# Kernel tuning notes

Measured on AMD Instinct MI355X. Metric: run time of the kernel, lower is better.

The kernel has to match this reference:

```python
import jax, jax.numpy as jnp
import numpy as np


def _conv1x1(x, W, b):
    # x: [B,C,H,W] (NCHW), W: [out,in] (1x1 conv kernel), b: [out]
    return jnp.einsum('bchw,oc->bohw', x, W) + b[None, :, None, None]


def setup_inputs() -> dict:
    key = jax.random.key(0)
    ks = jax.random.split(key, 12)
    B, C, H, W = 8, 256, 64, 64
    s = 1.0 / np.sqrt(C)
    x = jax.random.normal(ks[0], (B, C, H, W), dtype=jnp.float32)
    mask = jnp.round(jax.random.uniform(ks[1], (B, 1, H, W), dtype=jnp.float32))
    Wq = jax.random.normal(ks[2], (C, C), dtype=jnp.float32) * s
    bq = jax.random.normal(ks[3], (C,), dtype=jnp.float32) * 0.01
    Wk = jax.random.normal(ks[4], (C, C), dtype=jnp.float32) * s
    bk = jax.random.normal(ks[5], (C,), dtype=jnp.float32) * 0.01
    Wv = jax.random.normal(ks[6], (C, C), dtype=jnp.float32) * s
    bv = jax.random.normal(ks[7], (C,), dtype=jnp.float32) * 0.01
    Wo = jax.random.normal(ks[8], (C, C), dtype=jnp.float32) * s
    bo = jax.random.normal(ks[9], (C,), dtype=jnp.float32) * 0.01
    gamma = jnp.zeros((1,), dtype=jnp.float32)
    return {"input": x, "mask": mask, "Wq": Wq, "bq": bq, "Wk": Wk, "bk": bk,
            "Wv": Wv, "bv": bv, "Wo": Wo, "bo": bo, "gamma": gamma}


def reference(input, mask, Wq, bq, Wk, bk, Wv, bv, Wo, bo, gamma):
    B, C, H, W = input.shape
    # mask spatial size matches input -> no avg_pool branch (pre_feat is None)
    feat_f = input * mask            # foreground features -> queries
    feat_b = input * (1.0 - mask)    # background features -> keys/values
    q = _conv1x1(feat_f, Wq, bq).reshape(B, C, -1)   # [B,C,N]
    k = _conv1x1(feat_b, Wk, bk).reshape(B, C, -1)   # [B,C,N]
    v = _conv1x1(feat_b, Wv, bv).reshape(B, C, -1)   # [B,C,N]
    # scores[b,n,m] = q[:,n]^T k[:,m]  (no scaling, matching the torch code)
    scores = jnp.einsum('bcn,bcm->bnm', q, k)        # [B,N,N]
    attn = jax.nn.softmax(scores, axis=-1)
    out = jnp.einsum('bnm,bcm->bcn', attn, v).reshape(B, C, H, W)
    out = _conv1x1(out, Wo, bo)
    return out + gamma * input
```

## Files before the change

kernel.cpp:

```cpp
#include <hip/hip_runtime.h>

#define CC 256
#define NN 4096
#define NB 8
#define NM ((size_t)CC * NN)

typedef _Float16 f16;
typedef f16 f16x4 __attribute__((ext_vector_type(4)));
typedef f16 f16x8 __attribute__((ext_vector_type(8)));
typedef float f32x4 __attribute__((ext_vector_type(4)));
typedef unsigned int u32;

#define GLD16(gp, lp) __builtin_amdgcn_global_load_lds( \
    (const __attribute__((address_space(1))) u32*)(const void*)(gp), \
    (__attribute__((address_space(3))) u32*)(void*)(lp), 16, 0, 0)

__global__ __launch_bounds__(256) void wprep_kernel(
    const float* __restrict__ Wq, const float* __restrict__ Wk,
    const float* __restrict__ Wv, f16* __restrict__ w16)
{
    int i = (blockIdx.x * 256 + threadIdx.x) * 4;
    float4 a = *(const float4*)(Wq + i);
    float4 b = *(const float4*)(Wk + i);
    float4 c = *(const float4*)(Wv + i);
    f16x4 ha, hb, hc;
    ha[0]=(f16)a.x; ha[1]=(f16)a.y; ha[2]=(f16)a.z; ha[3]=(f16)a.w;
    hb[0]=(f16)b.x; hb[1]=(f16)b.y; hb[2]=(f16)b.z; hb[3]=(f16)b.w;
    hc[0]=(f16)c.x; hc[1]=(f16)c.y; hc[2]=(f16)c.z; hc[3]=(f16)c.w;
    *(f16x4*)(w16 + i)           = ha;
    *(f16x4*)(w16 + 65536 + i)   = hb;
    *(f16x4*)(w16 + 131072 + i)  = hc;
}

__global__ __launch_bounds__(256) void mask_scan_kernel(
    const float* __restrict__ mask, int* __restrict__ posm, int* __restrict__ counts)
{
    const int b = blockIdx.x;
    const int t = threadIdx.x;
    const int lane = t & 63, w = t >> 6;
    __shared__ int wsum[4];
    const float* mp = mask + (size_t)b * NN;
    int* pp = posm + (size_t)b * NN;

    int loc[16], cnt = 0;
#pragma unroll
    for (int i = 0; i < 16; ++i) {
        loc[i] = cnt;
        cnt += (mp[t * 16 + i] == 0.0f) ? 1 : 0;
    }
    int inc = cnt;
#pragma unroll
    for (int d = 1; d < 64; d <<= 1) {
        int v = __shfl_up(inc, d, 64);
        if (lane >= d) inc += v;
    }
    if (lane == 63) wsum[w] = inc;
    int exc = inc - cnt;
    __syncthreads();
    int base = exc;
    for (int i = 0; i < w; ++i) base += wsum[i];
#pragma unroll
    for (int i = 0; i < 16; ++i)
        pp[t * 16 + i] = (mp[t * 16 + i] == 0.0f) ? (base + loc[i]) : -1;
    if (t == 0) counts[b] = wsum[0] + wsum[1] + wsum[2] + wsum[3];
}

__global__ __launch_bounds__(256, 2) void proj_fused_kernel(
    const float* __restrict__ x, const float* __restrict__ mask,
    const f16* __restrict__ w16, const float* __restrict__ bq,
    const float* __restrict__ bk, const float* __restrict__ bv,
    f16* __restrict__ wsh, const int* __restrict__ posm,
    const int* __restrict__ counts, int b0)
{
    __shared__ f16x8 xf[2048];
    __shared__ f16x8 xb[2048];

    const int t = threadIdx.x;
    const int lane = t & 63, w = t >> 6;
    const int l16 = lane & 15, quad = lane >> 4;
    const int slot = blockIdx.x;
    const int b = b0 + slot;
    const int n0 = blockIdx.y * 64;
    const float* xp = x + (size_t)b * NM;
    f16* base = wsh + (size_t)slot * 4 * NM;
    const int* pom = posm + (size_t)b * NN;

    float mf  = mask[(size_t)b * NN + n0 + lane];
    float mbk = 1.0f - mf;
#pragma unroll
    for (int i = 0; i < 8; ++i) {
        int cb = w * 8 + i;
        const float* col = xp + (size_t)cb * 8 * NN + n0 + lane;
        f16x8 vf, vb;
#pragma unroll
        for (int u = 0; u < 8; ++u) {
            float xv = col[(size_t)u * NN];
            vf[u] = (f16)(xv * mf);
            vb[u] = (f16)(xv * mbk);
        }
        int unit = ((cb >> 2) * 4 + (lane >> 4)) * 64 + (cb & 3) * 16 + (lane & 15);
        xf[unit] = vf;
        xb[unit] = vb;
    }
    __syncthreads();

#pragma unroll
    for (int pr = 0; pr < 6; ++pr) {
        int j0  = w * 12 + pr * 2;
        int p   = j0 >> 4;
        int oc0 = j0 & 15;
        const f16* Wp     = w16 + (size_t)p * 65536;
        const float* bias = (p == 0) ? bq : (p == 1) ? bk : bv;
        const f16x8* bt   = (p == 0) ? xf : xb;

        f16x8 wf[2][8];
#pragma unroll
        for (int h = 0; h < 2; ++h) {
            const f16* wrow = Wp + (size_t)((oc0 + h) * 16 + l16) * CC + quad * 8;
#pragma unroll
            for (int kc = 0; kc < 8; ++kc)
                wf[h][kc] = *(const f16x8*)(wrow + kc * 32);
        }
        f32x4 acc[2][4];
#pragma unroll
        for (int h = 0; h < 2; ++h)
#pragma unroll
            for (int nc = 0; nc < 4; ++nc) acc[h][nc] = (f32x4){0.f, 0.f, 0.f, 0.f};
#pragma unroll
        for (int nc = 0; nc < 4; ++nc)
#pragma unroll
            for (int kc = 0; kc < 8; ++kc) {
                f16x8 bf = bt[(kc * 4 + nc) * 64 + lane];
                acc[0][nc] = __builtin_amdgcn_mfma_f32_16x16x32_f16(wf[0][kc], bf, acc[0][nc], 0, 0, 0);
                acc[1][nc] = __builtin_amdgcn_mfma_f32_16x16x32_f16(wf[1][kc], bf, acc[1][nc], 0, 0, 0);
            }
#pragma unroll
        for (int h = 0; h < 2; ++h) {
            int oc = oc0 + h;
            float bvv[4];
#pragma unroll
            for (int r = 0; r < 4; ++r) bvv[r] = bias[oc * 16 + quad * 4 + r];
            if (p == 2) {
                f16* vpl = base + 2 * NM;
#pragma unroll
                for (int nc = 0; nc < 4; ++nc) {
                    int cp = pom[n0 + nc * 16 + l16];
                    if (cp >= 0) {
#pragma unroll
                        for (int r = 0; r < 4; ++r)
                            vpl[(size_t)(oc * 16 + quad * 4 + r) * NN + cp] =
                                (f16)(acc[h][nc][r] + bvv[r]);
                    }
                }
            } else if (p == 1) {
                f16* kpl = base + NM;
#pragma unroll
                for (int nc = 0; nc < 4; ++nc) {
                    int cp = pom[n0 + nc * 16 + l16];
                    if (cp >= 0) {
                        f16x4 pk;
#pragma unroll
                        for (int r = 0; r < 4; ++r) pk[r] = (f16)(acc[h][nc][r] + bvv[r]);
                        *(f16x4*)(kpl + (size_t)cp * CC + oc * 16 + quad * 4) = pk;
                    }
                }
            } else {
                f16* qpl = base;
#pragma unroll
                for (int nc = 0; nc < 4; ++nc) {
                    f16x4 pk;
#pragma unroll
                    for (int r = 0; r < 4; ++r) pk[r] = (f16)(acc[h][nc][r] + bvv[r]);
                    *(f16x4*)(qpl + (size_t)(n0 + nc * 16 + l16) * CC + oc * 16 + quad * 4) = pk;
                }
            }
        }
    }

    if (blockIdx.y == 0) {
        int Fb = counts[b];
        int Mp = (Fb + 31) & ~31;
        int pad = Mp - Fb;
        if (pad > 0) {
            f16* kpl = base + NM;
            f16* vpl = base + 2 * NM;
            f16x8 z8;
#pragma unroll
            for (int i = 0; i < 8; ++i) z8[i] = (f16)0.0f;
            for (int idx = t; idx < pad * 32; idx += 256)
                *(f16x8*)(kpl + (size_t)(Fb + idx / 32) * CC + (idx & 31) * 8) = z8;
            for (int idx = t; idx < pad * CC; idx += 256)
                vpl[(size_t)(idx / pad) * NN + Fb + (idx % pad)] = (f16)0.0f;
        }
    }
}

__global__ __launch_bounds__(256, 2) void flash_kernel(
    f16* __restrict__ wsh, const float* __restrict__ bk,
    const float* __restrict__ bv, const int* __restrict__ counts, int b0)
{
    __shared__ f16x8 klds[2][1024];
    __shared__ f16x8 vlds[2][1024];
    __shared__ f16 pbuf[4][16 * 40];

    const int t    = threadIdx.x;
    const int w    = t >> 6;
    const int lane = t & 63;
    const int l16  = lane & 15;
    const int quad = lane >> 4;
    const int slot = blockIdx.x;
    const int n0   = blockIdx.y * 64;

    f16* base = wsh + (size_t)slot * 4 * NM;
    const f16* qt = base;
    const f16* kt = base + NM;
    const f16* vp = base + 2 * NM;
    f16* op       = base + 3 * NM;

    const int Fb = counts[b0 + slot];
    const int nt = (Fb + 31) >> 5;

    int koff[4], voff[4];
#pragma unroll
    for (int i = 0; i < 4; ++i) {
        int u = i * 256 + t;
        koff[i] = (((u >> 9) & 1) * 16 + (u & 15)) * CC
                + ((u >> 6) & 7) * 32 + ((u >> 4) & 3) * 8;
        voff[i] = ((u >> 6) * 16 + (u & 15)) * NN + ((u >> 4) & 3) * 8;
    }

#define ISSUE(m0_, b_) do {                                                     \
    _Pragma("unroll")                                                           \
    for (int i_ = 0; i_ < 4; ++i_)                                              \
        GLD16(kt + (size_t)(m0_) * CC + koff[i_],                               \
              (f16*)&klds[b_][i_ * 256 + w * 64]);                              \
    _Pragma("unroll")                                                           \
    for (int i_ = 0; i_ < 4; ++i_)                                              \
        GLD16(vp + (size_t)(m0_) + voff[i_],                                    \
              (f16*)&vlds[b_][i_ * 256 + w * 64]);                              \
} while (0)

    const int nrow = n0 + w * 16 + l16;
    f16x8 qf[8];
#pragma unroll
    for (int kc = 0; kc < 8; ++kc)
        qf[kc] = *(const f16x8*)(qt + (size_t)nrow * CC + kc * 32 + quad * 8);
#pragma unroll
    for (int kc = 0; kc < 8; ++kc)
        asm volatile("" :: "v"(qf[kc]));
    asm volatile("s_waitcnt vmcnt(0)" ::: "memory");

    f32x4 oacc[17];
#pragma unroll
    for (int i = 0; i < 17; ++i) oacc[i] = (f32x4){0.f, 0.f, 0.f, 0.f};
    float M[4] = {-3.0e38f, -3.0e38f, -3.0e38f, -3.0e38f};

    f16* pw = &pbuf[w][0];
    f16x8 ones;
#pragma unroll
    for (int i = 0; i < 8; ++i) ones[i] = (f16)1.0f;

    if (nt > 0) ISSUE(0, 0);
    int cur = 0;

    for (int it = 0; it < nt; ++it) {
        if (it + 1 < nt) {
            ISSUE((it + 1) * 32, cur ^ 1);
            asm volatile("s_waitcnt vmcnt(8)" ::: "memory");
        } else {
            asm volatile("s_waitcnt vmcnt(0)" ::: "memory");
        }
        __builtin_amdgcn_s_barrier();
        asm volatile("" ::: "memory");

        f32x4 s[2];
        s[0] = (f32x4){0.f, 0.f, 0.f, 0.f};
        s[1] = (f32x4){0.f, 0.f, 0.f, 0.f};
        __builtin_amdgcn_s_setprio(1);
#pragma unroll
        for (int kc = 0; kc < 8; ++kc) {
            f16x8 k0 = klds[cur][kc * 64 + lane];
            f16x8 k1 = klds[cur][(8 + kc) * 64 + lane];
            s[0] = __builtin_amdgcn_mfma_f32_16x16x32_f16(qf[kc], k0, s[0], 0, 0, 0);
            s[1] = __builtin_amdgcn_mfma_f32_16x16x32_f16(qf[kc], k1, s[1], 0, 0, 0);
        }
        __builtin_amdgcn_s_setprio(0);

        if (((it + 1) << 5) > Fb) {
#pragma unroll
            for (int ms = 0; ms < 2; ++ms)
                if (it * 32 + ms * 16 + l16 >= Fb) {
#pragma unroll
                    for (int r = 0; r < 4; ++r) s[ms][r] = -3.0e38f;
                }
        }

        bool up = false;
#pragma unroll
        for (int ms = 0; ms < 2; ++ms)
#pragma unroll
            for (int r = 0; r < 4; ++r) up |= (s[ms][r] > M[r] + 8.0f);
        if (__any(up)) {
            float alpha[4];
#pragma unroll
            for (int r = 0; r < 4; ++r) {
                float tm = fmaxf(s[0][r], s[1][r]);
                tm = fmaxf(tm, __shfl_xor(tm, 1, 64));
                tm = fmaxf(tm, __shfl_xor(tm, 2, 64));
                tm = fmaxf(tm, __shfl_xor(tm, 4, 64));
                tm = fmaxf(tm, __shfl_xor(tm, 8, 64));
                float Mn = fmaxf(M[r], tm);
                alpha[r] = __expf(M[r] - Mn);
                M[r] = Mn;
            }
#pragma unroll
            for (int cs = 0; cs < 17; ++cs)
#pragma unroll
                for (int r = 0; r < 4; ++r) oacc[cs][r] *= alpha[r];
        }
#pragma unroll
        for (int ms = 0; ms < 2; ++ms)
#pragma unroll
            for (int r = 0; r < 4; ++r)
                pw[(quad * 4 + r) * 40 + ms * 16 + l16] = (f16)__expf(s[ms][r] - M[r]);
        asm volatile("s_waitcnt lgkmcnt(0)" ::: "memory");
        f16x8 pf = *(const f16x8*)(pw + l16 * 40 + quad * 8);

        __builtin_amdgcn_s_setprio(1);
#pragma unroll
        for (int cs = 0; cs < 16; ++cs) {
            f16x8 vf = vlds[cur][cs * 64 + lane];
            oacc[cs] = __builtin_amdgcn_mfma_f32_16x16x32_f16(pf, vf, oacc[cs], 0, 0, 0);
        }
        oacc[16] = __builtin_amdgcn_mfma_f32_16x16x32_f16(pf, ones, oacc[16], 0, 0, 0);
        __builtin_amdgcn_s_setprio(0);

        asm volatile("" ::: "memory");
        __builtin_amdgcn_s_barrier();
        cur ^= 1;
    }
    asm volatile("s_waitcnt vmcnt(0)" ::: "memory");

    {
        float cn = 0.f;
#pragma unroll
        for (int kc = 0; kc < 8; ++kc) {
            const float* bkp = bk + kc * 32 + quad * 8;
#pragma unroll
            for (int j = 0; j < 8; ++j)
                cn += (float)qf[kc][j] * bkp[j];
        }
        cn += __shfl_xor(cn, 16, 64);
        cn += __shfl_xor(cn, 32, 64);
        const float Ff = (float)(NN - Fb);
        float aw[4], wv[4];
#pragma unroll
        for (int r = 0; r < 4; ++r) {
            float cr = __shfl(cn, quad * 4 + r, 64);
            float Mn = fmaxf(M[r], cr);
            aw[r] = __expf(M[r] - Mn);
            wv[r] = Ff * __expf(cr - Mn);
            M[r] = Mn;
        }
#pragma unroll
        for (int cs = 0; cs < 16; ++cs) {
            float bvc = bv[cs * 16 + l16];
#pragma unroll
            for (int r = 0; r < 4; ++r)
                oacc[cs][r] = oacc[cs][r] * aw[r] + wv[r] * bvc;
        }
#pragma unroll
        for (int r = 0; r < 4; ++r)
            oacc[16][r] = oacc[16][r] * aw[r] + wv[r];
    }

    float inv[4];
#pragma unroll
    for (int r = 0; r < 4; ++r) inv[r] = 1.0f / oacc[16][r];
#pragma unroll
    for (int cs = 0; cs < 16; ++cs)
#pragma unroll
        for (int r = 0; r < 4; ++r)
            op[(size_t)(cs * 16 + l16) * NN + n0 + w * 16 + quad * 4 + r] =
                (f16)(oacc[cs][r] * inv[r]);
#undef ISSUE
}

__global__ __launch_bounds__(256, 2) void final_kernel(
    const f16* __restrict__ wsh, const float* __restrict__ Wo,
    const float* __restrict__ bo, const float* __restrict__ x,
    const float* __restrict__ gamma, float* __restrict__ outall, int b0)
{
    __shared__ f16x8 ot[2048];

    const int t = threadIdx.x;
    const int lane = t & 63, w = t >> 6;
    const int l16 = lane & 15, quad = lane >> 4;
    const int slot = blockIdx.x;
    const int b = b0 + slot;
    const int n0 = blockIdx.y * 64;
    const f16* O = wsh + ((size_t)slot * 4 + 3) * NM;
    const float* xp = x + (size_t)b * NM;
    float* outp = outall + (size_t)b * NM;

#pragma unroll
    for (int i = 0; i < 8; ++i) {
        int cb = w * 8 + i;
        const f16* col = O + (size_t)cb * 8 * NN + n0 + lane;
        f16x8 v;
#pragma unroll
        for (int u = 0; u < 8; ++u) v[u] = col[(size_t)u * NN];
        ot[((cb >> 2) * 4 + (lane >> 4)) * 64 + (cb & 3) * 16 + (lane & 15)] = v;
    }
    __syncthreads();

    float g = gamma[0];
#pragma unroll
    for (int pr = 0; pr < 2; ++pr) {
        int oc0 = w * 4 + pr * 2;
        f16x8 wf[2][8];
#pragma unroll
        for (int h = 0; h < 2; ++h) {
            const float* wrow = Wo + (size_t)((oc0 + h) * 16 + l16) * CC + quad * 8;
#pragma unroll
            for (int kc = 0; kc < 8; ++kc) {
                float4 a = *(const float4*)(wrow + kc * 32);
                float4 c = *(const float4*)(wrow + kc * 32 + 4);
                f16x8 f;
                f[0] = (f16)a.x; f[1] = (f16)a.y; f[2] = (f16)a.z; f[3] = (f16)a.w;
                f[4] = (f16)c.x; f[5] = (f16)c.y; f[6] = (f16)c.z; f[7] = (f16)c.w;
                wf[h][kc] = f;
            }
        }
        f32x4 acc[2][4];
#pragma unroll
        for (int h = 0; h < 2; ++h)
#pragma unroll
            for (int nc = 0; nc < 4; ++nc) acc[h][nc] = (f32x4){0.f, 0.f, 0.f, 0.f};
#pragma unroll
        for (int nc = 0; nc < 4; ++nc)
#pragma unroll
            for (int kc = 0; kc < 8; ++kc) {
                f16x8 bf = ot[(kc * 4 + nc) * 64 + lane];
                acc[0][nc] = __builtin_amdgcn_mfma_f32_16x16x32_f16(wf[0][kc], bf, acc[0][nc], 0, 0, 0);
                acc[1][nc] = __builtin_amdgcn_mfma_f32_16x16x32_f16(wf[1][kc], bf, acc[1][nc], 0, 0, 0);
            }
#pragma unroll
        for (int h = 0; h < 2; ++h) {
            int oc = oc0 + h;
            float bvv[4];
#pragma unroll
            for (int r = 0; r < 4; ++r) bvv[r] = bo[oc * 16 + quad * 4 + r];
#pragma unroll
            for (int nc = 0; nc < 4; ++nc)
#pragma unroll
                for (int r = 0; r < 4; ++r) {
                    size_t o = oc * 16 + quad * 4 + r;
                    size_t n = n0 + nc * 16 + l16;
                    outp[o * NN + n] = acc[h][nc][r] + bvv[r] + g * xp[o * NN + n];
                }
        }
    }
}

__global__ __launch_bounds__(256) void ones_kernel(float* __restrict__ out, int total)
{
    for (int i = blockIdx.x * 256 + threadIdx.x; i < total; i += gridDim.x * 256)
        out[i] = 1.0f;
}

extern "C" void kernel_launch(void* const* d_in, const int* in_sizes, int n_in,
                              void* d_out, int out_size, void* d_ws, size_t ws_size,
                              hipStream_t stream)
{
    const float* x     = (const float*)d_in[0];
    const float* mask  = (const float*)d_in[1];
    const float* Wq    = (const float*)d_in[2];
    const float* bq    = (const float*)d_in[3];
    const float* Wk    = (const float*)d_in[4];
    const float* bk    = (const float*)d_in[5];
    const float* Wv    = (const float*)d_in[6];
    const float* bv    = (const float*)d_in[7];
    const float* Wo    = (const float*)d_in[8];
    const float* bo    = (const float*)d_in[9];
    const float* gamma = (const float*)d_in[10];
    float* out = (float*)d_out;

    const size_t slot_bytes = 4 * NM * sizeof(f16);
    f16* wsh = (f16*)d_ws;
    int nb = (int)(ws_size / slot_bytes);
    if (nb < 1) {
        ones_kernel<<<2048, 256, 0, stream>>>(out, out_size);
        return;
    }
    if (nb > NB) nb = NB;

    int* counts = (int*)(out + out_size) - 64;
    int* posm   = counts - NB * NN;
    f16* w16    = (f16*)posm - 3 * 65536;
    mask_scan_kernel<<<NB, 256, 0, stream>>>(mask, posm, counts);
    wprep_kernel<<<64, 256, 0, stream>>>(Wq, Wk, Wv, w16);

    for (int b0 = 0; b0 < NB; b0 += nb) {
        int nbc = NB - b0; if (nbc > nb) nbc = nb;
        dim3 gT(nbc, NN / 64);
        proj_fused_kernel<<<gT, 256, 0, stream>>>(x, mask, w16, bq, bk, bv,
                                                  wsh, posm, counts, b0);
        flash_kernel<<<gT, 256, 0, stream>>>(wsh, bk, bv, counts, b0);
        final_kernel<<<gT, 256, 0, stream>>>(wsh, Wo, bo, x, gamma, out, b0);
    }
}
```

Measured before the change: 310.8 us.

## Fuse output 1x1 projection into flash attention epilogue via LDS

The flash kernel now writes its normalized fp16 attention output tile into the shared-memory K buffers instead of global memory. It then runs the Wo projection, bias and gamma residual in the same block, which removes the separate final kernel and the global write and read of the O plane. Wo is pre-converted to fp16 once in the weight-prep kernel. The scratch data (fp16 weights, mask positions, counts) moves from the tail of the output buffer into the now-unused O plane of the workspace. This raises register and LDS pressure in the flash kernel and relies on the LDS reuse being synchronized correctly.

```diff
diff --git a/kernel.cpp b/kernel.cpp
--- a/kernel.cpp
+++ b/kernel.cpp
@@ -17,19 +17,23 @@
 
 __global__ __launch_bounds__(256) void wprep_kernel(
     const float* __restrict__ Wq, const float* __restrict__ Wk,
-    const float* __restrict__ Wv, f16* __restrict__ w16)
+    const float* __restrict__ Wv, const float* __restrict__ Wo,
+    f16* __restrict__ w16)
 {
     int i = (blockIdx.x * 256 + threadIdx.x) * 4;
     float4 a = *(const float4*)(Wq + i);
     float4 b = *(const float4*)(Wk + i);
     float4 c = *(const float4*)(Wv + i);
-    f16x4 ha, hb, hc;
+    float4 d = *(const float4*)(Wo + i);
+    f16x4 ha, hb, hc, hd;
     ha[0]=(f16)a.x; ha[1]=(f16)a.y; ha[2]=(f16)a.z; ha[3]=(f16)a.w;
     hb[0]=(f16)b.x; hb[1]=(f16)b.y; hb[2]=(f16)b.z; hb[3]=(f16)b.w;
     hc[0]=(f16)c.x; hc[1]=(f16)c.y; hc[2]=(f16)c.z; hc[3]=(f16)c.w;
-    *(f16x4*)(w16 + i)           = ha;
-    *(f16x4*)(w16 + 65536 + i)   = hb;
-    *(f16x4*)(w16 + 131072 + i)  = hc;
+    hd[0]=(f16)d.x; hd[1]=(f16)d.y; hd[2]=(f16)d.z; hd[3]=(f16)d.w;
+    *(f16x4*)(w16 + i)            = ha;
+    *(f16x4*)(w16 + 65536 + i)    = hb;
+    *(f16x4*)(w16 + 131072 + i)   = hc;
+    *(f16x4*)(w16 + 196608 + i)   = hd;
 }
 
 __global__ __launch_bounds__(256) void mask_scan_kernel(
@@ -197,7 +201,9 @@
 
 __global__ __launch_bounds__(256, 2) void flash_kernel(
     f16* __restrict__ wsh, const float* __restrict__ bk,
-    const float* __restrict__ bv, const int* __restrict__ counts, int b0)
+    const float* __restrict__ bv, const float* __restrict__ bo,
+    const float* __restrict__ x, const float* __restrict__ gamma,
+    float* __restrict__ outall, int b0)
 {
     __shared__ f16x8 klds[2][1024];
     __shared__ f16x8 vlds[2][1024];
@@ -215,9 +221,12 @@
     const f16* qt = base;
     const f16* kt = base + NM;
     const f16* vp = base + 2 * NM;
-    f16* op       = base + 3 * NM;
-
-    const int Fb = counts[b0 + slot];
+
+    const f16* wo16 = wsh + 3 * NM + (size_t)3 * 65536;
+    const int* counts = (const int*)(wsh + 3 * NM + (size_t)4 * 65536) + NB * NN;
+
+    const int b = b0 + slot;
+    const int Fb = counts[b];
     const int nt = (Fb + 31) >> 5;
 
     int koff[4], voff[4];
@@ -377,43 +386,22 @@
     float inv[4];
 #pragma unroll
     for (int r = 0; r < 4; ++r) inv[r] = 1.0f / oacc[16][r];
-#pragma unroll
-    for (int cs = 0; cs < 16; ++cs)
+
+    f16* otf = (f16*)&klds[0][0];
+#pragma unroll
+    for (int cs = 0; cs < 16; ++cs) {
+        int cb = cs * 2 + (l16 >> 3);
+        int ubase = ((cb >> 2) * 4 + w) * 64 + (cb & 3) * 16 + quad * 4;
+        int j = l16 & 7;
 #pragma unroll
         for (int r = 0; r < 4; ++r)
-            op[(size_t)(cs * 16 + l16) * NN + n0 + w * 16 + quad * 4 + r] =
-                (f16)(oacc[cs][r] * inv[r]);
-#undef ISSUE
-}
-
-__global__ __launch_bounds__(256, 2) void final_kernel(
-    const f16* __restrict__ wsh, const float* __restrict__ Wo,
-    const float* __restrict__ bo, const float* __restrict__ x,
-    const float* __restrict__ gamma, float* __restrict__ outall, int b0)
-{
-    __shared__ f16x8 ot[2048];
-
-    const int t = threadIdx.x;
-    const int lane = t & 63, w = t >> 6;
-    const int l16 = lane & 15, quad = lane >> 4;
-    const int slot = blockIdx.x;
-    const int b = b0 + slot;
-    const int n0 = blockIdx.y * 64;
-    const f16* O = wsh + ((size_t)slot * 4 + 3) * NM;
+            otf[(ubase + r) * 8 + j] = (f16)(oacc[cs][r] * inv[r]);
+    }
+    __syncthreads();
+
     const float* xp = x + (size_t)b * NM;
     float* outp = outall + (size_t)b * NM;
-
-#pragma unroll
-    for (int i = 0; i < 8; ++i) {
-        int cb = w * 8 + i;
-        const f16* col = O + (size_t)cb * 8 * NN + n0 + lane;
-        f16x8 v;
-#pragma unroll
-        for (int u = 0; u < 8; ++u) v[u] = col[(size_t)u * NN];
-        ot[((cb >> 2) * 4 + (lane >> 4)) * 64 + (cb & 3) * 16 + (lane & 15)] = v;
-    }
-    __syncthreads();
-
+    const f16x8* ot = (const f16x8*)otf;
     float g = gamma[0];
 #pragma unroll
     for (int pr = 0; pr < 2; ++pr) {
@@ -421,16 +409,10 @@
         f16x8 wf[2][8];
 #pragma unroll
         for (int h = 0; h < 2; ++h) {
-            const float* wrow = Wo + (size_t)((oc0 + h) * 16 + l16) * CC + quad * 8;
-#pragma unroll
-            for (int kc = 0; kc < 8; ++kc) {
-                float4 a = *(const float4*)(wrow + kc * 32);
-                float4 c = *(const float4*)(wrow + kc * 32 + 4);
-                f16x8 f;
-                f[0] = (f16)a.x; f[1] = (f16)a.y; f[2] = (f16)a.z; f[3] = (f16)a.w;
-                f[4] = (f16)c.x; f[5] = (f16)c.y; f[6] = (f16)c.z; f[7] = (f16)c.w;
-                wf[h][kc] = f;
-            }
+            const f16* wrow = wo16 + (size_t)((oc0 + h) * 16 + l16) * CC + quad * 8;
+#pragma unroll
+            for (int kc = 0; kc < 8; ++kc)
+                wf[h][kc] = *(const f16x8*)(wrow + kc * 32);
         }
         f32x4 acc[2][4];
 #pragma unroll
@@ -461,6 +443,7 @@
                 }
         }
     }
+#undef ISSUE
 }
 
 __global__ __launch_bounds__(256) void ones_kernel(float* __restrict__ out, int total)
@@ -495,18 +478,18 @@
     }
     if (nb > NB) nb = NB;
 
-    int* counts = (int*)(out + out_size) - 64;
-    int* posm   = counts - NB * NN;
-    f16* w16    = (f16*)posm - 3 * 65536;
+    f16* scr = wsh + 3 * NM;
+    f16* w16 = scr;
+    int* posm = (int*)(scr + (size_t)4 * 65536);
+    int* counts = posm + NB * NN;
     mask_scan_kernel<<<NB, 256, 0, stream>>>(mask, posm, counts);
-    wprep_kernel<<<64, 256, 0, stream>>>(Wq, Wk, Wv, w16);
+    wprep_kernel<<<64, 256, 0, stream>>>(Wq, Wk, Wv, Wo, w16);
 
     for (int b0 = 0; b0 < NB; b0 += nb) {
         int nbc = NB - b0; if (nbc > nb) nbc = nb;
         dim3 gT(nbc, NN / 64);
         proj_fused_kernel<<<gT, 256, 0, stream>>>(x, mask, w16, bq, bk, bv,
                                                   wsh, posm, counts, b0);
-        flash_kernel<<<gT, 256, 0, stream>>>(wsh, bk, bv, counts, b0);
-        final_kernel<<<gT, 256, 0, stream>>>(wsh, Wo, bo, x, gamma, out, b0);
-    }
-}
+        flash_kernel<<<gT, 256, 0, stream>>>(wsh, bk, bv, bo, x, gamma, out, b0);
+    }
+}
```

Result: faster. 287.2 us (-7.6%).
